# Kernel optimization log

Measured on AMD Instinct MI355X. Metric: run time of the kernel, lower is better.

Reference implementation:

```python
import jax, jax.numpy as jnp
import numpy as np

H = 16          # n_heads
DN = 128        # qk_nope_head_dim
DR = 64         # qk_rope_head_dim
DV = 128        # v_head_dim
R = 512         # kv_lora_rank
DIM = 2048
THETA = 10000.0
EPS = 1e-6
SCALE = (DN + DR) ** -0.5


def rms_norm(x, w):
    var = jnp.mean(x * x, axis=-1, keepdims=True)
    return x * jax.lax.rsqrt(var + EPS) * w


def rope_cos_sin(seqlen):
    # DeepSeek freqs: 1/theta^(2i/d) over adjacent pairs
    inv = 1.0 / (THETA ** (jnp.arange(0, DR, 2, dtype=jnp.float32) / DR))  # [DR/2]
    ang = jnp.arange(seqlen, dtype=jnp.float32)[:, None] * inv             # [s, DR/2]
    return jnp.cos(ang), jnp.sin(ang)


def apply_rope(t, cos, sin):
    # t: [b, s, h, DR]; rotate adjacent pairs (complex multiply)
    b, s, h, d = t.shape
    t = t.reshape(b, s, h, d // 2, 2)
    x0, x1 = t[..., 0], t[..., 1]
    c = cos[None, :, None, :]
    sn = sin[None, :, None, :]
    out = jnp.stack([x0 * c - x1 * sn, x0 * sn + x1 * c], axis=-1)
    return out.reshape(b, s, h, d)


def setup_inputs() -> dict:
    key = jax.random.key(0)
    ks = jax.random.split(key, 6)
    b, s = 2, 2048
    sc = lambda n: n ** -0.5
    return {
        "x": jax.random.normal(ks[0], (b, s, DIM), jnp.float32),
        "wq": jax.random.normal(ks[1], (DIM, H * (DN + DR)), jnp.float32) * sc(DIM),
        "wkv_a": jax.random.normal(ks[2], (DIM, R + DR), jnp.float32) * sc(DIM),
        "kv_norm_w": jnp.ones((R,), jnp.float32),
        "wkv_b": jax.random.normal(ks[3], (R, H * (DN + DV)), jnp.float32) * sc(R),
        "wo": jax.random.normal(ks[4], (H * DV, DIM), jnp.float32) * sc(H * DV),
    }


def reference(x, wq, wkv_a, kv_norm_w, wkv_b, wo):
    b, s, _ = x.shape
    cos, sin = rope_cos_sin(s)

    # Query projection (q_lora_rank == 0 -> direct)
    q = (x @ wq).reshape(b, s, H, DN + DR)
    q_nope, q_pe = q[..., :DN], q[..., DN:]
    q_pe = apply_rope(q_pe, cos, sin)

    # Compressed KV + decoupled rope key
    kv_a = x @ wkv_a                      # [b, s, R+DR]
    kv, k_pe = kv_a[..., :R], kv_a[..., R:]
    k_pe = apply_rope(k_pe[:, :, None, :], cos, sin)  # [b, s, 1, DR]
    kv = rms_norm(kv, kv_norm_w)
    kvb = (kv @ wkv_b).reshape(b, s, H, DN + DV)
    k_nope, v = kvb[..., :DN], kvb[..., DN:]

    qf = jnp.concatenate([q_nope, q_pe], axis=-1)                         # [b,s,H,192]
    kf = jnp.concatenate([k_nope, jnp.broadcast_to(k_pe, (b, s, H, DR))], axis=-1)

    scores = jnp.einsum("bshd,bthd->bhst", qf, kf) * SCALE
    mask = jnp.tril(jnp.ones((s, s), bool))
    scores = jnp.where(mask[None, None], scores, jnp.finfo(scores.dtype).min)
    p = jax.nn.softmax(scores, axis=-1)
    out = jnp.einsum("bhst,bthd->bshd", p, v).reshape(b, s, H * DV)
    return out @ wo
```

## Files before the change

kernel.cpp:

```cpp
#include <hip/hip_runtime.h>
#include <hip/hip_bf16.h>
#include <math.h>

#define NB 2
#define NS 2048
#define ND 2048
#define NH 16
#define DNOPE 128
#define DROPE 64
#define DVAL 128
#define RANK 512
#define QW (NH*(DNOPE+DROPE))
#define AW (RANK+DROPE)
#define AWPAD 640
#define BW (NH*(DNOPE+DVAL))
#define OW (NH*DVAL)
#define ATT_SCALE2 0.10411758590510176f
#define LOG2_10000 13.287712379549449f

typedef __attribute__((ext_vector_type(8))) short short8;
typedef __attribute__((ext_vector_type(4))) float f32x4;

__device__ __forceinline__ float b2f(unsigned short u) {
  unsigned x = ((unsigned)u) << 16; float f; __builtin_memcpy(&f, &x, 4); return f;
}
__device__ __forceinline__ unsigned short f2b(float f) {
  unsigned x; __builtin_memcpy(&x, &f, 4);
  unsigned r = (x + 0x7fffu + ((x >> 16) & 1u)) >> 16;
  return (unsigned short)r;
}
__device__ __forceinline__ unsigned cvtpk(float a, float b) {
  unsigned r;
  asm("v_cvt_pk_bf16_f32 %0, %1, %2" : "=v"(r) : "v"(a), "v"(b));
  return r;
}
__device__ __forceinline__ void gload16(const void* g, void* lds) {
  __builtin_amdgcn_global_load_lds((const __attribute__((address_space(1))) void*)g,
                                   (__attribute__((address_space(3))) void*)lds, 16, 0, 0);
}

__global__ __launch_bounds__(256) void k_cvt(const float* __restrict__ X,
                                             unsigned short* __restrict__ Y) {
  long i = ((long)blockIdx.x * 256 + threadIdx.x) * 4;
  float4 v = *(const float4*)(X + i);
  ushort4 o;
  o.x = f2b(v.x); o.y = f2b(v.y); o.z = f2b(v.z); o.w = f2b(v.w);
  *(ushort4*)(Y + i) = o;
}

__global__ __launch_bounds__(256) void k_transpose(const float* __restrict__ W,
                                                   unsigned short* __restrict__ WT,
                                                   int K, int N) {
  __shared__ float t[32][33];
  const int k0 = blockIdx.x * 32, n0 = blockIdx.y * 32;
  const int tx = threadIdx.x & 31, ty = threadIdx.x >> 5;
  #pragma unroll
  for (int i = 0; i < 32; i += 8) {
    int n = n0 + tx;
    float v = (n < N) ? W[(size_t)(k0 + ty + i) * N + n] : 0.f;
    t[ty + i][tx] = v;
  }
  __syncthreads();
  #pragma unroll
  for (int i = 0; i < 32; i += 8)
    WT[(size_t)(n0 + ty + i) * K + k0 + tx] = f2b(t[tx][ty + i]);
}

template <typename OutT>
__global__ __launch_bounds__(256) void gemm_bf16(
    const unsigned short* __restrict__ A, const unsigned short* __restrict__ BT,
    OutT* __restrict__ C, int M, int N, int K, int lda) {
  __shared__ short8 AsV[1024];
  __shared__ short8 BsV[1024];
  const int tid = threadIdx.x;
  const int l = tid & 63, w = tid >> 6;
  const int nwg = gridDim.x * gridDim.y;
  const int bid = blockIdx.y * gridDim.x + blockIdx.x;
  const int sbid = (bid & 7) * (nwg >> 3) + (bid >> 3);
  const int bx = sbid % gridDim.x, by = sbid / gridDim.x;
  const int bm = by * 128, bn = bx * 128;
  const int wm = (w >> 1) * 64, wn = (w & 1) * 64;
  f32x4 acc[4][4] = {};

  const int srow = tid >> 3;
  const int gk   = ((((tid & 7) * 16) ^ ((srow & 7) << 4)) >> 1);
  const int sw   = l & 7;

  for (int k0 = 0; k0 < K; k0 += 64) {
    #pragma unroll
    for (int i = 0; i < 4; ++i) {
      const int row = i * 32 + srow;
      gload16(A + (size_t)(bm + row) * lda + k0 + gk, (char*)AsV + i * 4096 + w * 1024);
      gload16(BT + (size_t)(bn + row) * K   + k0 + gk, (char*)BsV + i * 4096 + w * 1024);
    }
    __syncthreads();
    #pragma unroll
    for (int kk2 = 0; kk2 < 2; ++kk2) {
      const int kb = kk2 * 4 + (l >> 4);
      short8 af[4], bg[4];
      #pragma unroll
      for (int mi = 0; mi < 4; ++mi)
        af[mi] = AsV[(wm + mi * 16 + (l & 15)) * 8 + (kb ^ sw)];
      #pragma unroll
      for (int ni = 0; ni < 4; ++ni)
        bg[ni] = BsV[(wn + ni * 16 + (l & 15)) * 8 + (kb ^ sw)];
      #pragma unroll
      for (int mi = 0; mi < 4; ++mi)
        #pragma unroll
        for (int ni = 0; ni < 4; ++ni)
          acc[mi][ni] = __builtin_amdgcn_mfma_f32_16x16x32_bf16(af[mi], bg[ni], acc[mi][ni], 0, 0, 0);
    }
    __syncthreads();
  }

  const int r0 = bm + wm + (l >> 4) * 4;
  const int c0 = bn + wn + (l & 15);
  #pragma unroll
  for (int mi = 0; mi < 4; ++mi)
    #pragma unroll
    for (int ni = 0; ni < 4; ++ni) {
      const int col = c0 + ni * 16;
      if (col < N) {
        #pragma unroll
        for (int j = 0; j < 4; ++j) {
          float v = acc[mi][ni][j];
          if constexpr (__is_same(OutT, float))
            C[(size_t)(r0 + mi * 16 + j) * N + col] = v;
          else
            C[(size_t)(r0 + mi * 16 + j) * N + col] = f2b(v);
        }
      }
    }
}

__global__ __launch_bounds__(256) void gemm_fused_qkva(
    const unsigned short* __restrict__ A, const unsigned short* __restrict__ BT,
    unsigned short* __restrict__ Cq, unsigned short* __restrict__ Ckva, int K) {
  __shared__ short8 AsV[1024];
  __shared__ short8 BsV[1024];
  const int tid = threadIdx.x;
  const int l = tid & 63, w = tid >> 6;
  const int nwg = gridDim.x * gridDim.y;
  const int bid = blockIdx.y * gridDim.x + blockIdx.x;
  const int sbid = (bid & 7) * (nwg >> 3) + (bid >> 3);
  const int bx = sbid % gridDim.x, by = sbid / gridDim.x;
  const int bm = by * 128, bn = bx * 128;
  const int wm = (w >> 1) * 64, wn = (w & 1) * 64;
  f32x4 acc[4][4] = {};

  const int srow = tid >> 3;
  const int gk   = ((((tid & 7) * 16) ^ ((srow & 7) << 4)) >> 1);
  const int sw   = l & 7;

  for (int k0 = 0; k0 < K; k0 += 64) {
    #pragma unroll
    for (int i = 0; i < 4; ++i) {
      const int row = i * 32 + srow;
      gload16(A + (size_t)(bm + row) * K + k0 + gk, (char*)AsV + i * 4096 + w * 1024);
      gload16(BT + (size_t)(bn + row) * K + k0 + gk, (char*)BsV + i * 4096 + w * 1024);
    }
    __syncthreads();
    #pragma unroll
    for (int kk2 = 0; kk2 < 2; ++kk2) {
      const int kb = kk2 * 4 + (l >> 4);
      short8 af[4], bg[4];
      #pragma unroll
      for (int mi = 0; mi < 4; ++mi)
        af[mi] = AsV[(wm + mi * 16 + (l & 15)) * 8 + (kb ^ sw)];
      #pragma unroll
      for (int ni = 0; ni < 4; ++ni)
        bg[ni] = BsV[(wn + ni * 16 + (l & 15)) * 8 + (kb ^ sw)];
      #pragma unroll
      for (int mi = 0; mi < 4; ++mi)
        #pragma unroll
        for (int ni = 0; ni < 4; ++ni)
          acc[mi][ni] = __builtin_amdgcn_mfma_f32_16x16x32_bf16(af[mi], bg[ni], acc[mi][ni], 0, 0, 0);
    }
    __syncthreads();
  }

  const int r0 = bm + wm + (l >> 4) * 4;
  const int c0 = bn + wn + (l & 15);
  #pragma unroll
  for (int mi = 0; mi < 4; ++mi)
    #pragma unroll
    for (int ni = 0; ni < 4; ++ni) {
      const int col = c0 + ni * 16;
      #pragma unroll
      for (int j = 0; j < 4; ++j) {
        const float v = acc[mi][ni][j];
        const int row = r0 + mi * 16 + j;
        if (col < QW)
          Cq[(size_t)row * QW + col] = f2b(v);
        else if (col - QW < AW)
          Ckva[(size_t)row * AW + (col - QW)] = f2b(v);
      }
    }
}

__global__ __launch_bounds__(64) void k_rms_ropek(unsigned short* __restrict__ kva,
                                                  const float* __restrict__ w) {
  const int row = blockIdx.x;
  const int t = row & (NS - 1);
  const int lane = threadIdx.x;
  unsigned short* p = kva + (long)row * AW;

  short8 v = *(const short8*)(p + lane * 8);
  float f[8];
  float ss = 0.f;
  #pragma unroll
  for (int j = 0; j < 8; ++j) {
    f[j] = b2f((unsigned short)v[j]);
    ss += f[j] * f[j];
  }
  #pragma unroll
  for (int o2 = 1; o2 < 64; o2 <<= 1) ss += __shfl_xor(ss, o2, 64);
  const float sc = rsqrtf(ss / (float)RANK + 1e-6f);
  short8 ov;
  #pragma unroll
  for (int j = 0; j < 8; ++j)
    ov[j] = (short)f2b(f[j] * sc * w[lane * 8 + j]);
  *(short8*)(p + lane * 8) = ov;

  if (lane < 32) {
    const float invf = exp2f(-(float)lane * (LOG2_10000 / 32.0f));
    const float ang = (float)t * invf;
    float s, c;
    sincosf(ang, &s, &c);
    unsigned short* pp = p + RANK + 2 * lane;
    const float x0 = b2f(pp[0]), x1 = b2f(pp[1]);
    pp[0] = f2b(x0 * c - x1 * s);
    pp[1] = f2b(x0 * s + x1 * c);
  }
}

__global__ __launch_bounds__(512) void k_ropeq_b(unsigned short* __restrict__ q) {
  const int row = blockIdx.x;
  const int t = row & (NS - 1);
  const int h = threadIdx.x >> 5;
  const int i = threadIdx.x & 31;
  const float invf = exp2f(-(float)i * (LOG2_10000 / 32.0f));
  const float ang = (float)t * invf;
  float s, c;
  sincosf(ang, &s, &c);
  unsigned short* p = q + (long)row * QW + h * (DNOPE + DROPE) + DNOPE + 2 * i;
  const float x0 = b2f(p[0]), x1 = b2f(p[1]);
  p[0] = f2b(x0 * c - x1 * s);
  p[1] = f2b(x0 * s + x1 * c);
}

#define KBLK 64
#define KSL 24
#define VTS 72
#define VBUF (DVAL*VTS)
#define PLS 72
#define QTILES (NS/128)
__global__ __launch_bounds__(512) void k_attn_mfma(
    const unsigned short* __restrict__ qg,
    const unsigned short* __restrict__ kvbg,
    const unsigned short* __restrict__ kvag,
    unsigned short* __restrict__ attg) {
  __shared__ short8 Ks[KBLK * KSL];
  __shared__ __align__(16) unsigned short VT[2 * VBUF];
  __shared__ __align__(16) unsigned short Pl[128 * PLS];
  const int tid = threadIdx.x;
  const int l = tid & 63, w = tid >> 6;
  const int g = l >> 4, r16 = l & 15;
  const int h = blockIdx.y;
  const int b = blockIdx.z;
  const unsigned short* q   = qg   + (size_t)b * NS * QW;
  const unsigned short* kvb = kvbg + (size_t)b * NS * BW;
  const unsigned short* kva = kvag + (size_t)b * NS * AW;
  unsigned short* att = attg + (size_t)b * NS * OW;

  const unsigned short* kbs[3]; int kstp[3]; char* kdst[3];
  #pragma unroll
  for (int i = 0; i < 3; ++i) {
    const int chunk = i * 512 + tid;
    const int row = chunk / KSL, p = chunk % KSL;
    const int s = (p & ~7) | ((p & 7) ^ (row & 7));
    const int d0 = s * 8;
    if (d0 < DNOPE) { kbs[i] = kvb + (size_t)row * BW + h * 256 + d0; kstp[i] = KBLK * BW; }
    else            { kbs[i] = kva + (size_t)row * AW + RANK + (d0 - DNOPE); kstp[i] = KBLK * AW; }
    kdst[i] = (char*)Ks + (size_t)(i * 512 + (tid & ~63)) * 16;
  }
  const int vt_t = tid >> 3, vqd = tid & 7;
  const unsigned short* vbs = kvb + (size_t)vt_t * BW + h * 256 + DNOPE + vqd * 8;
  unsigned short* vwd = VT + (vqd * 8) * VTS + (vt_t ^ (vqd << 3));

  #pragma unroll 1
  for (int phase = 0; phase < 2; ++phase) {
    const int qt = phase ? (QTILES - 1 - (int)blockIdx.x) : (int)blockIdx.x;
    const int nt = 2 * qt + 2;
    const int qrow0 = qt * 128 + w * 16;

    short8 aq[6];
    {
      const unsigned short* qp = q + (size_t)(qrow0 + r16) * QW + h * 192 + g * 8;
      #pragma unroll
      for (int f = 0; f < 6; ++f) aq[f] = *(const short8*)(qp + f * 32);
    }
    f32x4 o[8] = {};
    float m_j[4], l_j[4];
    #pragma unroll
    for (int j = 0; j < 4; ++j) { m_j[j] = -1e30f; l_j[j] = 0.f; }

    const unsigned short* kq0 = kbs[0];
    const unsigned short* kq1 = kbs[1];
    const unsigned short* kq2 = kbs[2];
    const unsigned short* vq  = vbs;

    gload16(kq0, kdst[0]); kq0 += kstp[0];
    gload16(kq1, kdst[1]); kq1 += kstp[1];
    gload16(kq2, kdst[2]); kq2 += kstp[2];
    {
      short8 vA = *(const short8*)(vq);
      short8 vB = *(const short8*)(vq + 64);
      #pragma unroll
      for (int jj = 0; jj < 8; ++jj) {
        vwd[jj * VTS] = (unsigned short)vA[jj];
        vwd[64 * VTS + jj * VTS] = (unsigned short)vB[jj];
      }
      vq += KBLK * BW;
    }
    __syncthreads();
    int cur = 0;

    for (int kt = 0; kt < nt; ++kt) {
      f32x4 sa[4] = {};
      __builtin_amdgcn_s_setprio(1);
      #pragma unroll
      for (int f = 0; f < 6; ++f) {
        #pragma unroll
        for (int n = 0; n < 4; ++n) {
          const int row = n * 16 + r16;
          const int s = f * 4 + g;
          const int phys = (s & ~7) | ((s & 7) ^ (row & 7));
          short8 bg = Ks[row * KSL + phys];
          sa[n] = __builtin_amdgcn_mfma_f32_16x16x32_bf16(aq[f], bg, sa[n], 0, 0, 0);
        }
      }
      __builtin_amdgcn_s_setprio(0);
      __syncthreads();

      const bool pref = (kt + 1 < nt);
      short8 vA, vB;
      if (pref) {
        gload16(kq0, kdst[0]); kq0 += kstp[0];
        gload16(kq1, kdst[1]); kq1 += kstp[1];
        gload16(kq2, kdst[2]); kq2 += kstp[2];
        vA = *(const short8*)(vq);
        vB = *(const short8*)(vq + 64);
        vq += KBLK * BW;
      }

      const bool diag = (kt >= nt - 2);
      float pj[4][4];
      #pragma unroll
      for (int n = 0; n < 4; ++n) {
        const int key = kt * KBLK + n * 16 + r16;
        #pragma unroll
        for (int j = 0; j < 4; ++j) {
          float v = sa[n][j] * ATT_SCALE2;
          if (diag && key > (qrow0 + g * 4 + j)) v = -1e30f;
          pj[n][j] = v;
        }
      }
      float mjl[4];
      #pragma unroll
      for (int j = 0; j < 4; ++j)
        mjl[j] = fmaxf(fmaxf(pj[0][j], pj[1][j]), fmaxf(pj[2][j], pj[3][j]));
      const bool myneed = (mjl[0] > m_j[0] + 8.f) | (mjl[1] > m_j[1] + 8.f) |
                          (mjl[2] > m_j[2] + 8.f) | (mjl[3] > m_j[3] + 8.f);
      if (__any(myneed)) {
        #pragma unroll
        for (int j = 0; j < 4; ++j) {
          float mx = mjl[j];
          #pragma unroll
          for (int o2 = 1; o2 < 16; o2 <<= 1) mx = fmaxf(mx, __shfl_xor(mx, o2, 64));
          const float mn = fmaxf(m_j[j], mx);
          const float c = exp2f(m_j[j] - mn);
          l_j[j] *= c;
          #pragma unroll
          for (int n8 = 0; n8 < 8; ++n8) o[n8][j] *= c;
          m_j[j] = mn;
        }
      }
      #pragma unroll
      for (int j = 0; j < 4; ++j) {
        float p0 = exp2f(pj[0][j] - m_j[j]);
        float p1 = exp2f(pj[1][j] - m_j[j]);
        float p2 = exp2f(pj[2][j] - m_j[j]);
        float p3 = exp2f(pj[3][j] - m_j[j]);
        l_j[j] += (p0 + p1) + (p2 + p3);
        const int prow = w * 16 + g * 4 + j;
        const unsigned pk01 = cvtpk(p0, p1);
        const unsigned pk23 = cvtpk(p2, p3);
        Pl[prow * PLS +  0 + r16] = (unsigned short)pk01;
        Pl[prow * PLS + 16 + r16] = (unsigned short)(pk01 >> 16);
        Pl[prow * PLS + 32 + r16] = (unsigned short)pk23;
        Pl[prow * PLS + 48 + r16] = (unsigned short)(pk23 >> 16);
      }

      if (pref) {
        unsigned short* dst = vwd + (cur ^ 1) * VBUF;
        #pragma unroll
        for (int jj = 0; jj < 8; ++jj) {
          dst[jj * VTS] = (unsigned short)vA[jj];
          dst[64 * VTS + jj * VTS] = (unsigned short)vB[jj];
        }
      }

      const int hb = r16 >> 3;
      const unsigned short* vbase = VT + cur * VBUF;
      #pragma unroll
      for (int kk = 0; kk < 2; ++kk) {
        short8 pa = *(const short8*)&Pl[(w * 16 + r16) * PLS + kk * 32 + g * 8];
        __builtin_amdgcn_s_setprio(1);
        #pragma unroll
        for (int n8 = 0; n8 < 8; ++n8) {
          const int blk = (kk * 4 + g) ^ ((n8 * 2 + hb) & 7);
          short8 vb = *(const short8*)&vbase[(n8 * 16 + r16) * VTS + blk * 8];
          o[n8] = __builtin_amdgcn_mfma_f32_16x16x32_bf16(pa, vb, o[n8], 0, 0, 0);
        }
        __builtin_amdgcn_s_setprio(0);
      }
      __syncthreads();
      cur ^= 1;
    }

    #pragma unroll
    for (int j = 0; j < 4; ++j) {
      float ls = l_j[j];
      #pragma unroll
      for (int o2 = 1; o2 < 16; o2 <<= 1) ls += __shfl_xor(ls, o2, 64);
      const float inv = 1.0f / ls;
      const size_t rowoff = (size_t)(qrow0 + g * 4 + j) * OW + h * DVAL;
      #pragma unroll
      for (int n8 = 0; n8 < 8; ++n8)
        att[rowoff + n8 * 16 + r16] = f2b(o[n8][j] * inv);
    }
    __syncthreads();
  }
}

extern "C" void kernel_launch(void* const* d_in, const int* in_sizes, int n_in,
                              void* d_out, int out_size, void* d_ws, size_t ws_size,
                              hipStream_t stream) {
  const float* x      = (const float*)d_in[0];
  const float* wq     = (const float*)d_in[1];
  const float* wkv_a  = (const float*)d_in[2];
  const float* w_norm = (const float*)d_in[3];
  const float* wkv_b  = (const float*)d_in[4];
  const float* wo     = (const float*)d_in[5];
  float* out = (float*)d_out;

  unsigned short* wqT   = (unsigned short*)d_ws;
  unsigned short* wkvaT = wqT   + (long)QW * ND;
  unsigned short* wkvbT = wkvaT + (long)AWPAD * ND;
  unsigned short* woT   = wkvbT + (long)BW * RANK;
  unsigned short* xb2   = woT   + (long)ND * OW;
  unsigned short* q2    = xb2   + (long)NB * NS * ND;
  unsigned short* kva2  = q2    + (long)NB * NS * QW;
  unsigned short* kvb2  = kva2  + (long)NB * NS * AW;
  unsigned short* att2  = xb2;

  k_transpose<<<dim3(ND / 32, QW / 32),    dim3(256), 0, stream>>>(wq,    wqT,   ND,  QW);
  k_transpose<<<dim3(ND / 32, AWPAD / 32), dim3(256), 0, stream>>>(wkv_a, wkvaT, ND,  AW);
  k_transpose<<<dim3(RANK / 32, BW / 32),  dim3(256), 0, stream>>>(wkv_b, wkvbT, RANK, BW);
  k_transpose<<<dim3(OW / 32, ND / 32),    dim3(256), 0, stream>>>(wo,    woT,   OW,  ND);

  k_cvt<<<dim3((NB * NS * ND) / 1024), dim3(256), 0, stream>>>(x, xb2);
  gemm_fused_qkva<<<dim3((QW + AWPAD) / 128, (NB * NS) / 128), dim3(256), 0, stream>>>(
      xb2, wqT, q2, kva2, ND);
  k_rms_ropek<<<dim3(NB * NS), dim3(64), 0, stream>>>(kva2, w_norm);
  k_ropeq_b<<<dim3(NB * NS), dim3(512), 0, stream>>>(q2);
  gemm_bf16<unsigned short><<<dim3(BW / 128, (NB * NS) / 128), dim3(256), 0, stream>>>(
      kva2, wkvbT, kvb2, NB * NS, BW, RANK, AW);
  k_attn_mfma<<<dim3(QTILES / 2, NH, NB), dim3(512), 0, stream>>>(q2, kvb2, kva2, att2);
  gemm_bf16<float><<<dim3(ND / 128, (NB * NS) / 128), dim3(256), 0, stream>>>(
      att2, woT, out, NB * NS, ND, OW, OW);
}
```

Before: 293.8 us.

## Fuse query RoPE into attention and double-buffer K tiles in LDS

Removes the separate query RoPE kernel launch and instead rotates the rope part of each query fragment in registers as it is loaded inside the attention kernel. K tiles are now double-buffered in shared memory, so the next tile is prefetched at the start of each iteration and one __syncthreads per iteration is dropped. This saves a full read-modify-write pass over q and a launch, and lets loads overlap compute. In exchange it uses more LDS, which may lower occupancy, and adds sincos work per attention block.

```diff
diff --git a/kernel.cpp b/kernel.cpp
--- a/kernel.cpp
+++ b/kernel.cpp
@@ -234,23 +234,9 @@
   }
 }
 
-__global__ __launch_bounds__(512) void k_ropeq_b(unsigned short* __restrict__ q) {
-  const int row = blockIdx.x;
-  const int t = row & (NS - 1);
-  const int h = threadIdx.x >> 5;
-  const int i = threadIdx.x & 31;
-  const float invf = exp2f(-(float)i * (LOG2_10000 / 32.0f));
-  const float ang = (float)t * invf;
-  float s, c;
-  sincosf(ang, &s, &c);
-  unsigned short* p = q + (long)row * QW + h * (DNOPE + DROPE) + DNOPE + 2 * i;
-  const float x0 = b2f(p[0]), x1 = b2f(p[1]);
-  p[0] = f2b(x0 * c - x1 * s);
-  p[1] = f2b(x0 * s + x1 * c);
-}
-
 #define KBLK 64
 #define KSL 24
+#define KSB (KBLK*KSL*16)
 #define VTS 72
 #define VBUF (DVAL*VTS)
 #define PLS 72
@@ -260,7 +246,7 @@
     const unsigned short* __restrict__ kvbg,
     const unsigned short* __restrict__ kvag,
     unsigned short* __restrict__ attg) {
-  __shared__ short8 Ks[KBLK * KSL];
+  __shared__ short8 Ks[2 * KBLK * KSL];
   __shared__ __align__(16) unsigned short VT[2 * VBUF];
   __shared__ __align__(16) unsigned short Pl[128 * PLS];
   const int tid = threadIdx.x;
@@ -273,7 +259,7 @@
   const unsigned short* kva = kvag + (size_t)b * NS * AW;
   unsigned short* att = attg + (size_t)b * NS * OW;
 
-  const unsigned short* kbs[3]; int kstp[3]; char* kdst[3];
+  const unsigned short* kbs[3]; int kstp[3]; int kdo[3];
   #pragma unroll
   for (int i = 0; i < 3; ++i) {
     const int chunk = i * 512 + tid;
@@ -282,7 +268,7 @@
     const int d0 = s * 8;
     if (d0 < DNOPE) { kbs[i] = kvb + (size_t)row * BW + h * 256 + d0; kstp[i] = KBLK * BW; }
     else            { kbs[i] = kva + (size_t)row * AW + RANK + (d0 - DNOPE); kstp[i] = KBLK * AW; }
-    kdst[i] = (char*)Ks + (size_t)(i * 512 + (tid & ~63)) * 16;
+    kdo[i] = (i * 512 + (tid & ~63)) * 16;
   }
   const int vt_t = tid >> 3, vqd = tid & 7;
   const unsigned short* vbs = kvb + (size_t)vt_t * BW + h * 256 + DNOPE + vqd * 8;
@@ -297,8 +283,25 @@
     short8 aq[6];
     {
       const unsigned short* qp = q + (size_t)(qrow0 + r16) * QW + h * 192 + g * 8;
-      #pragma unroll
-      for (int f = 0; f < 6; ++f) aq[f] = *(const short8*)(qp + f * 32);
+      const float tpos = (float)(qrow0 + r16);
+      #pragma unroll
+      for (int f = 0; f < 6; ++f) {
+        short8 v = *(const short8*)(qp + f * 32);
+        if (f >= 4) {
+          const int ibase = (f - 4) * 16 + g * 4;
+          #pragma unroll
+          for (int m = 0; m < 4; ++m) {
+            const float invf = exp2f(-(float)(ibase + m) * (LOG2_10000 / 32.0f));
+            float s_, c_;
+            sincosf(tpos * invf, &s_, &c_);
+            const float x0 = b2f((unsigned short)v[2 * m]);
+            const float x1 = b2f((unsigned short)v[2 * m + 1]);
+            v[2 * m]     = (short)f2b(x0 * c_ - x1 * s_);
+            v[2 * m + 1] = (short)f2b(x0 * s_ + x1 * c_);
+          }
+        }
+        aq[f] = v;
+      }
     }
     f32x4 o[8] = {};
     float m_j[4], l_j[4];
@@ -310,9 +313,9 @@
     const unsigned short* kq2 = kbs[2];
     const unsigned short* vq  = vbs;
 
-    gload16(kq0, kdst[0]); kq0 += kstp[0];
-    gload16(kq1, kdst[1]); kq1 += kstp[1];
-    gload16(kq2, kdst[2]); kq2 += kstp[2];
+    gload16(kq0, (char*)Ks + kdo[0]); kq0 += kstp[0];
+    gload16(kq1, (char*)Ks + kdo[1]); kq1 += kstp[1];
+    gload16(kq2, (char*)Ks + kdo[2]); kq2 += kstp[2];
     {
       short8 vA = *(const short8*)(vq);
       short8 vB = *(const short8*)(vq + 64);
@@ -327,6 +330,19 @@
     int cur = 0;
 
     for (int kt = 0; kt < nt; ++kt) {
+      const bool pref = (kt + 1 < nt);
+      short8 vA, vB;
+      if (pref) {
+        char* kb1 = (char*)Ks + (cur ^ 1) * KSB;
+        gload16(kq0, kb1 + kdo[0]); kq0 += kstp[0];
+        gload16(kq1, kb1 + kdo[1]); kq1 += kstp[1];
+        gload16(kq2, kb1 + kdo[2]); kq2 += kstp[2];
+        vA = *(const short8*)(vq);
+        vB = *(const short8*)(vq + 64);
+        vq += KBLK * BW;
+      }
+
+      const short8* ksrc = Ks + cur * (KBLK * KSL);
       f32x4 sa[4] = {};
       __builtin_amdgcn_s_setprio(1);
       #pragma unroll
@@ -336,23 +352,11 @@
           const int row = n * 16 + r16;
           const int s = f * 4 + g;
           const int phys = (s & ~7) | ((s & 7) ^ (row & 7));
-          short8 bg = Ks[row * KSL + phys];
+          short8 bg = ksrc[row * KSL + phys];
           sa[n] = __builtin_amdgcn_mfma_f32_16x16x32_bf16(aq[f], bg, sa[n], 0, 0, 0);
         }
       }
       __builtin_amdgcn_s_setprio(0);
-      __syncthreads();
-
-      const bool pref = (kt + 1 < nt);
-      short8 vA, vB;
-      if (pref) {
-        gload16(kq0, kdst[0]); kq0 += kstp[0];
-        gload16(kq1, kdst[1]); kq1 += kstp[1];
-        gload16(kq2, kdst[2]); kq2 += kstp[2];
-        vA = *(const short8*)(vq);
-        vB = *(const short8*)(vq + 64);
-        vq += KBLK * BW;
-      }
 
       const bool diag = (kt >= nt - 2);
       float pj[4][4];
@@ -425,6 +429,7 @@
         }
         __builtin_amdgcn_s_setprio(0);
       }
+
       __syncthreads();
       cur ^= 1;
     }
@@ -474,7 +479,6 @@
   gemm_fused_qkva<<<dim3((QW + AWPAD) / 128, (NB * NS) / 128), dim3(256), 0, stream>>>(
       xb2, wqT, q2, kva2, ND);
   k_rms_ropek<<<dim3(NB * NS), dim3(64), 0, stream>>>(kva2, w_norm);
-  k_ropeq_b<<<dim3(NB * NS), dim3(512), 0, stream>>>(q2);
   gemm_bf16<unsigned short><<<dim3(BW / 128, (NB * NS) / 128), dim3(256), 0, stream>>>(
       kva2, wkvbT, kvb2, NB * NS, BW, RANK, AW);
   k_attn_mfma<<<dim3(QTILES / 2, NH, NB), dim3(512), 0, stream>>>(q2, kvb2, kva2, att2);
```

After: 293.4 us. About the same (-0.2%).
